# Optimization experiments

Hardware: AMD Instinct MI355X
Metric: run time of the kernel (lower is better)

Reference implementation:

```python
import jax, jax.numpy as jnp
import numpy as np

B, L, D, M = 32, 512, 768, 24  # batch, max_len, bert hidden, mentions per sample
MAX_SPAN = 16


def setup_inputs() -> dict:
    key = jax.random.key(0)
    k1, k2, k3, k4 = jax.random.split(key, 4)
    sequence_output = jax.random.normal(k1, (B, L, D), dtype=jnp.float32)
    head_indexes = jax.random.randint(k2, (B, L), 0, L)
    starts = jax.random.randint(k3, (B, M), 0, L - MAX_SPAN)
    lens = jax.random.randint(k4, (B, M), 1, MAX_SPAN)
    entity_mentions = jnp.stack([starts, starts + lens], axis=-1)  # [B, M, 2], start < end
    return {
        "sequence_output": sequence_output,
        "head_indexes": head_indexes,
        "entity_mentions": entity_mentions,
    }


def reference(sequence_output, head_indexes, entity_mentions):
    b, l, d = sequence_output.shape
    m = entity_mentions.shape[1]

    # per-sample head-token gather: seq[i] = seq[i][head_indexes[i]]
    seq = jnp.take_along_axis(sequence_output, head_indexes[..., None], axis=1)  # [B, L, D]

    # span mean-pool via exclusive prefix sums: mean(seq[s:e]) = (cs[e]-cs[s])/(e-s)
    cs = jnp.concatenate(
        [jnp.zeros((b, 1, d), seq.dtype), jnp.cumsum(seq, axis=1)], axis=1
    )  # [B, L+1, D]
    starts = entity_mentions[..., 0]  # [B, M]
    ends = entity_mentions[..., 1]    # [B, M]
    span_sum = (
        jnp.take_along_axis(cs, ends[..., None], axis=1)
        - jnp.take_along_axis(cs, starts[..., None], axis=1)
    )  # [B, M, D]
    pooled = span_sum / (ends - starts)[..., None].astype(seq.dtype)  # [B, M, D]

    # all ordered pairs i != j (eval path order: i outer, j inner, skip i==j)
    ii, jj = np.meshgrid(np.arange(m), np.arange(m), indexing="ij")
    offdiag = ii != jj
    ii = jnp.asarray(ii[offdiag])  # [P]
    jj = jnp.asarray(jj[offdiag])  # [P]
    p = ii.shape[0]

    obj = pooled[:, ii]  # [B, P, D]
    sub = pooled[:, jj]  # [B, P, D]
    relation_predictions = jnp.concatenate([obj, sub], axis=-1).reshape(b * p, 2 * d)

    batch_idx = jnp.repeat(jnp.arange(b), p)  # [B*P]
    pairs = jnp.stack(
        [
            batch_idx,
            starts[:, ii].reshape(-1),
            ends[:, ii].reshape(-1),
            starts[:, jj].reshape(-1),
            ends[:, jj].reshape(-1),
        ],
        axis=-1,
    )  # [B*P, 5] = [idx, obj_start, obj_end, subj_start, subj_end]
    return relation_predictions, pairs
```

## Files before the change

kernel.cpp:

```cpp
#include <hip/hip_runtime.h>

#define B 32
#define L 512
#define D 768
#define M 24
#define P (M * (M - 1))
#define G2 (D / 2)

typedef float f32x2 __attribute__((ext_vector_type(2)));

__global__ void __launch_bounds__(G2, 7)
fused_kernel(const float* __restrict__ seq,
             const int*   __restrict__ head,
             const int*   __restrict__ em,
             float*       __restrict__ out)
{
    int blk  = blockIdx.x;
    int g    = ((blk >> 4) << 3) + (blk & 7);
    int half = (blk >> 3) & 1;
    int b    = g / M, m = g - b * M;
    int tq   = threadIdx.x;

    const float* seqb  = seq  + (size_t)b * L * D;
    const int*   headb = head + b * L;
    const int*   emb   = em   + b * M * 2;

    int s = emb[2 * m];
    int e = emb[2 * m + 1];
    int len = e - s;

    int hidx[15];
    #pragma unroll
    for (int r = 0; r < 15; ++r) {
        int l = s + r; l = (l < e) ? l : s;
        hidx[r] = headb[l];
    }
    f32x2 vv[15];
    #pragma unroll
    for (int r = 0; r < 15; ++r)
        vv[r] = ((const f32x2*)(seqb + (size_t)hidx[r] * D))[tq];
    f32x2 acc = (f32x2)(0.f);
    #pragma unroll
    for (int r = 0; r < 15; ++r)
        acc += (r < len) ? vv[r] : (f32x2)(0.f);
    f32x2 v = acc * (1.0f / (float)len);

    f32x2* outg = (f32x2*)out;
    size_t rowbase = (size_t)b * P;

    if (half == 0) {
        size_t q = (rowbase + (size_t)m * 23) * 768 + tq;
        #pragma unroll
        for (int r = 0; r < 23; ++r) {
            outg[q] = v;
            q += 768;
        }
        if (tq < 23) {
            int r = tq;
            int j = (r < m) ? r : r + 1;
            float* o = out + (size_t)B * P * 2 * D
                     + (rowbase + (size_t)m * 23 + r) * 5;
            o[0] = (float)b;
            o[1] = (float)s;
            o[2] = (float)e;
            o[3] = (float)emb[2 * j];
            o[4] = (float)emb[2 * j + 1];
        }
    } else {
        #pragma unroll
        for (int i = 0; i < M; ++i) {
            if (i == m) continue;
            int r = (m < i) ? m : m - 1;
            size_t row = rowbase + (size_t)i * 23 + r;
            outg[row * 768 + G2 + tq] = v;
        }
    }
}

extern "C" void kernel_launch(void* const* d_in, const int* in_sizes, int n_in,
                              void* d_out, int out_size, void* d_ws, size_t ws_size,
                              hipStream_t stream) {
    const float* seq  = (const float*)d_in[0];
    const int*   head = (const int*)d_in[1];
    const int*   em   = (const int*)d_in[2];
    float* out = (float*)d_out;

    fused_kernel<<<B * M * 2, G2, 0, stream>>>(seq, head, em, out);
}
```

Baseline: 25.82 us.

## Split span rows across thread halves and reduce via shared memory

Before, two blocks per mention each recomputed the full span mean over all 384 column pairs, doing the gather twice. Now each block covers half the columns, and its two thread halves each gather alternate span rows. The partial sums are combined through shared memory, then one half writes the obj copies and the other writes the sub copies. This removes the duplicated gather work and halves the per-thread load count, at the cost of a __syncthreads and a small shared buffer.

```diff
diff --git a/kernel.cpp b/kernel.cpp
--- a/kernel.cpp
+++ b/kernel.cpp
@@ -5,21 +5,25 @@
 #define D 768
 #define M 24
 #define P (M * (M - 1))
-#define G2 (D / 2)
 
 typedef float f32x2 __attribute__((ext_vector_type(2)));
 
-__global__ void __launch_bounds__(G2, 7)
+__global__ void __launch_bounds__(384, 8)
 fused_kernel(const float* __restrict__ seq,
              const int*   __restrict__ head,
              const int*   __restrict__ em,
              float*       __restrict__ out)
 {
-    int blk  = blockIdx.x;
-    int g    = ((blk >> 4) << 3) + (blk & 7);
-    int half = (blk >> 3) & 1;
-    int b    = g / M, m = g - b * M;
-    int tq   = threadIdx.x;
+    __shared__ f32x2 pool[2][192];
+
+    int blk   = blockIdx.x;
+    int g     = blk >> 1;
+    int chalf = blk & 1;
+    int b = g / M, m = g - b * M;
+    int t  = threadIdx.x;
+    int rp = (t >= 192);
+    int c  = t - rp * 192;
+    int col = chalf * 192 + c;
 
     const float* seqb  = seq  + (size_t)b * L * D;
     const int*   headb = head + b * L;
@@ -28,38 +32,43 @@
     int s = emb[2 * m];
     int e = emb[2 * m + 1];
     int len = e - s;
+    int cnt = (len - rp + 1) >> 1;
 
-    int hidx[15];
+    int hidx[8];
     #pragma unroll
-    for (int r = 0; r < 15; ++r) {
-        int l = s + r; l = (l < e) ? l : s;
+    for (int r = 0; r < 8; ++r) {
+        int l = s + rp + 2 * r;
+        l = (l < e) ? l : s;
         hidx[r] = headb[l];
     }
-    f32x2 vv[15];
+    f32x2 vv[8];
     #pragma unroll
-    for (int r = 0; r < 15; ++r)
-        vv[r] = ((const f32x2*)(seqb + (size_t)hidx[r] * D))[tq];
+    for (int r = 0; r < 8; ++r)
+        vv[r] = ((const f32x2*)(seqb + (size_t)hidx[r] * D))[col];
     f32x2 acc = (f32x2)(0.f);
     #pragma unroll
-    for (int r = 0; r < 15; ++r)
-        acc += (r < len) ? vv[r] : (f32x2)(0.f);
-    f32x2 v = acc * (1.0f / (float)len);
+    for (int r = 0; r < 8; ++r)
+        acc += (r < cnt) ? vv[r] : (f32x2)(0.f);
+
+    pool[rp][c] = acc;
+    __syncthreads();
+    f32x2 v = (pool[0][c] + pool[1][c]) * (1.0f / (float)len);
 
     f32x2* outg = (f32x2*)out;
     size_t rowbase = (size_t)b * P;
 
-    if (half == 0) {
-        size_t q = (rowbase + (size_t)m * 23) * 768 + tq;
+    if (rp == 0) {
+        size_t q = (rowbase + (size_t)m * 23) * 768 + col;
         #pragma unroll
         for (int r = 0; r < 23; ++r) {
             outg[q] = v;
             q += 768;
         }
-        if (tq < 23) {
-            int r = tq;
-            int j = (r < m) ? r : r + 1;
+        if (chalf == 0 && c < 23) {
+            int rr = c;
+            int j = (rr < m) ? rr : rr + 1;
             float* o = out + (size_t)B * P * 2 * D
-                     + (rowbase + (size_t)m * 23 + r) * 5;
+                     + (rowbase + (size_t)m * 23 + rr) * 5;
             o[0] = (float)b;
             o[1] = (float)s;
             o[2] = (float)e;
@@ -72,7 +81,7 @@
             if (i == m) continue;
             int r = (m < i) ? m : m - 1;
             size_t row = rowbase + (size_t)i * 23 + r;
-            outg[row * 768 + G2 + tq] = v;
+            outg[row * 768 + 384 + col] = v;
         }
     }
 }
@@ -85,5 +94,5 @@
     const int*   em   = (const int*)d_in[2];
     float* out = (float*)d_out;
 
-    fused_kernel<<<B * M * 2, G2, 0, stream>>>(seq, head, em, out);
+    fused_kernel<<<B * M * 2, 384, 0, stream>>>(seq, head, em, out);
 }
```

Result: no change. 25.56 us (-1.0%).

## Split into pooling kernel and coalesced row-wise relation pair expansion kernel

Applied to the files above, without the earlier changes.

Pooled span means are first computed once per mention into a workspace buffer, along with the pair index rows. A second kernel then writes the output one row at a time, using 16-byte vector stores, by reading obj/sub vectors from the workspace. This is meant to replace the scattered per-mention write pattern with contiguous streaming writes. The cost is an extra kernel launch and a small workspace round trip.

```diff
diff --git a/kernel.cpp b/kernel.cpp
--- a/kernel.cpp
+++ b/kernel.cpp
@@ -5,29 +5,30 @@
 #define D 768
 #define M 24
 #define P (M * (M - 1))
-#define G2 (D / 2)
+#define ROWS 16
+#define NROW (B * P)
 
 typedef float f32x2 __attribute__((ext_vector_type(2)));
+typedef float f32x4 __attribute__((ext_vector_type(4)));
 
-__global__ void __launch_bounds__(G2, 7)
-fused_kernel(const float* __restrict__ seq,
-             const int*   __restrict__ head,
-             const int*   __restrict__ em,
-             float*       __restrict__ out)
+__global__ void __launch_bounds__(384)
+pool_kernel(const float* __restrict__ seq,
+            const int*   __restrict__ head,
+            const int*   __restrict__ em,
+            float*       __restrict__ pooled,
+            float*       __restrict__ pout)
 {
-    int blk  = blockIdx.x;
-    int g    = ((blk >> 4) << 3) + (blk & 7);
-    int half = (blk >> 3) & 1;
-    int b    = g / M, m = g - b * M;
-    int tq   = threadIdx.x;
+    int g = blockIdx.x;
+    int b = g / M, m = g - b * M;
+    int t = threadIdx.x;
+
+    const int* emb = em + b * M * 2;
+    int s = emb[2 * m];
+    int e = emb[2 * m + 1];
+    int len = e - s;
 
     const float* seqb  = seq  + (size_t)b * L * D;
     const int*   headb = head + b * L;
-    const int*   emb   = em   + b * M * 2;
-
-    int s = emb[2 * m];
-    int e = emb[2 * m + 1];
-    int len = e - s;
 
     int hidx[15];
     #pragma unroll
@@ -38,42 +39,51 @@
     f32x2 vv[15];
     #pragma unroll
     for (int r = 0; r < 15; ++r)
-        vv[r] = ((const f32x2*)(seqb + (size_t)hidx[r] * D))[tq];
+        vv[r] = ((const f32x2*)(seqb + (size_t)hidx[r] * D))[t];
     f32x2 acc = (f32x2)(0.f);
     #pragma unroll
     for (int r = 0; r < 15; ++r)
         acc += (r < len) ? vv[r] : (f32x2)(0.f);
-    f32x2 v = acc * (1.0f / (float)len);
+    acc *= 1.0f / (float)len;
 
-    f32x2* outg = (f32x2*)out;
-    size_t rowbase = (size_t)b * P;
+    ((f32x2*)pooled)[(size_t)g * 384 + t] = acc;
 
-    if (half == 0) {
-        size_t q = (rowbase + (size_t)m * 23) * 768 + tq;
-        #pragma unroll
-        for (int r = 0; r < 23; ++r) {
-            outg[q] = v;
-            q += 768;
-        }
-        if (tq < 23) {
-            int r = tq;
-            int j = (r < m) ? r : r + 1;
-            float* o = out + (size_t)B * P * 2 * D
-                     + (rowbase + (size_t)m * 23 + r) * 5;
-            o[0] = (float)b;
-            o[1] = (float)s;
-            o[2] = (float)e;
-            o[3] = (float)emb[2 * j];
-            o[4] = (float)emb[2 * j + 1];
-        }
-    } else {
-        #pragma unroll
-        for (int i = 0; i < M; ++i) {
-            if (i == m) continue;
-            int r = (m < i) ? m : m - 1;
-            size_t row = rowbase + (size_t)i * 23 + r;
-            outg[row * 768 + G2 + tq] = v;
-        }
+    if (t < 23) {
+        int rr = t;
+        int j = (rr < m) ? rr : rr + 1;
+        float* o = pout + ((size_t)b * P + (size_t)m * 23 + rr) * 5;
+        o[0] = (float)b;
+        o[1] = (float)s;
+        o[2] = (float)e;
+        o[3] = (float)emb[2 * j];
+        o[4] = (float)emb[2 * j + 1];
+    }
+}
+
+__global__ void __launch_bounds__(384)
+rel_kernel(const float* __restrict__ pooled,
+           float*       __restrict__ out)
+{
+    int blk  = blockIdx.x;
+    int row0 = blk * ROWS;
+    int t    = threadIdx.x;
+    int hf   = t >= 192;
+    int tq   = t - 192 * hf;
+
+    const f32x4* pq   = (const f32x4*)pooled;
+    f32x4*       outq = (f32x4*)out;
+
+    #pragma unroll 4
+    for (int r = 0; r < ROWS; ++r) {
+        int row = row0 + r;
+        int b   = row / P;
+        int p   = row - b * P;
+        int i   = p / 23;
+        int rr  = p - i * 23;
+        int j   = (rr < i) ? rr : rr + 1;
+        int src = hf ? j : i;
+        f32x4 v = pq[(size_t)(b * M + src) * 192 + tq];
+        outq[(size_t)row * 384 + t] = v;
     }
 }
 
@@ -83,7 +93,10 @@
     const float* seq  = (const float*)d_in[0];
     const int*   head = (const int*)d_in[1];
     const int*   em   = (const int*)d_in[2];
-    float* out = (float*)d_out;
+    float* out    = (float*)d_out;
+    float* pooled = (float*)d_ws;
 
-    fused_kernel<<<B * M * 2, G2, 0, stream>>>(seq, head, em, out);
+    pool_kernel<<<B * M, 384, 0, stream>>>(seq, head, em, pooled,
+                                           out + (size_t)B * P * 2 * D);
+    rel_kernel<<<NROW / ROWS, 384, 0, stream>>>(pooled, out);
 }
```

New measurement: 32.75 us. +26.8%, slower.
